# Kernel optimization log

Hardware: AMD Instinct MI355X
Metric: run time of the kernel (lower is better)

The kernel has to match this reference:

```python
import jax, jax.numpy as jnp
import numpy as np


def setup_inputs() -> dict:
    key = jax.random.key(0)
    ks = jax.random.split(key, 5)
    B, M, R = 32, 32, 128
    d_lang, d_region, d_rank, d_fusion = 1024, 2048, 256, 256
    u = jax.random.normal(ks[0], (B, M, d_lang), dtype=jnp.float32)
    v = jax.random.normal(ks[1], (B, R, d_region), dtype=jnp.float32)
    # Linear weights stored torch-style as (out_features, in_features)
    Wu = jax.random.normal(ks[2], (d_rank, d_lang), dtype=jnp.float32) * (1.0 / np.sqrt(d_lang))
    Wv = jax.random.normal(ks[3], (d_rank, d_region), dtype=jnp.float32) * (1.0 / np.sqrt(d_region))
    Wp = jax.random.normal(ks[4], (d_fusion, d_rank), dtype=jnp.float32) * (1.0 / np.sqrt(d_rank))
    bp = jnp.zeros((d_fusion,), dtype=jnp.float32)
    return {"u": u, "v": v, "Wu": Wu, "Wv": Wv, "Wp": Wp, "bp": bp}


def reference(u, v, Wu, Wv, Wp, bp):
    # u: (B, M, d_lang), v: (B, R, d_region)
    up = jnp.einsum('bmd,rd->bmr', u, Wu)          # (B, M, d_rank)  [rd: out x in]
    vp = jnp.einsum('bnd,rd->bnr', v, Wv)          # (B, R, d_rank)
    # broadcast bilinear multiply: (B, M, R, d_rank)
    prod = up[:, :, None, :] * vp[:, None, :, :]
    o = jnp.einsum('bmnk,fk->bmnf', prod, Wp) + bp  # p-linear -> (B, M, R, d_fusion)
    # dropout is identity in inference mode
    return jax.nn.relu(o)
```

## Files before the change

### kernel.cpp

```cpp
#include <hip/hip_runtime.h>
#include <hip/hip_bf16.h>


typedef __attribute__((ext_vector_type(8))) short short8;
typedef __attribute__((ext_vector_type(4))) float floatx4;
typedef __attribute__((ext_vector_type(4))) unsigned uintx4;

__device__ __forceinline__ short f2bf(float f) {
    union { float f; unsigned u; } cv; cv.f = f;
    unsigned r = cv.u + 0x7fffu + ((cv.u >> 16) & 1u);
    return (short)(r >> 16);
}
__device__ __forceinline__ unsigned pack_rne(float x, float y) {
    __hip_bfloat162 h = __float22bfloat162_rn(make_float2(x, y));
    union { __hip_bfloat162 h; unsigned u; } cv; cv.h = h;
    return cv.u;
}
__device__ __forceinline__ unsigned scale2_rne(short a, short b, float ua, float ub) {
    float x = __uint_as_float(((unsigned)(unsigned short)a) << 16) * ua;
    float y = __uint_as_float(((unsigned)(unsigned short)b) << 16) * ub;
    return pack_rne(x, y);
}

#define MFMA16(a, b, c) __builtin_amdgcn_mfma_f32_16x16x32_bf16((a), (b), (c), 0, 0, 0)

__global__ __launch_bounds__(256) void proj_kernel(
    const float* __restrict__ u, const float* __restrict__ Wu,
    float* __restrict__ upf,
    const float* __restrict__ v, const float* __restrict__ Wv,
    short* __restrict__ vpb,
    const float* __restrict__ Wp, short* __restrict__ Wp_bf)
{
    __shared__ __align__(16) short Xs[2][32 * 64];
    __shared__ __align__(16) short Wsh[2][64 * 64];

    const int tid  = threadIdx.x;
    const int lane = tid & 63;
    const int wave = tid >> 6;
    const int quad = lane >> 4;
    const int l15  = lane & 15;

    const int bid = blockIdx.x;

    if (bid < 32) {
        const int widx = (bid * 256 + tid) * 8;
        float4 g0 = *(const float4*)(Wp + widx);
        float4 g1 = *(const float4*)(Wp + widx + 4);
        short8 o;
        o[0] = f2bf(g0.x); o[1] = f2bf(g0.y); o[2] = f2bf(g0.z); o[3] = f2bf(g0.w);
        o[4] = f2bf(g1.x); o[5] = f2bf(g1.y); o[6] = f2bf(g1.z); o[7] = f2bf(g1.w);
        *(short8*)(Wp_bf + widx) = o;
    }

    const int xcd = bid & 7, j = bid >> 3;
    const int cb  = j & 3;
    const int pidx = xcd + 8 * (j >> 2);
    const float *X, *W; int D, r0; bool is_u;
    if (pidx < 32) { is_u = true;  X = u; W = Wu; D = 1024; r0 = pidx * 32; }
    else           { is_u = false; X = v; W = Wv; D = 2048; r0 = (pidx - 32) * 32; }
    const int c0 = cb * 64;
    const int wr = (wave >> 1) * 16;
    const int wc = (wave & 1) * 32;

    const int xr_ = tid >> 3, xk = (tid & 7) * 8;
    const int wr_ = tid >> 2, wk = (tid & 3) * 16;
    const float* xg = X + (size_t)(r0 + xr_) * D + xk;
    const float* wg = W + (size_t)(c0 + wr_) * D + wk;
    const int xswz  = (xr_ & 7) << 4;
    const int wswz  = (wr_ & 7) << 4;
    const int xbase = xr_ * 128 + xk * 2;
    const int wbase = wr_ * 128 + wk * 2;

    floatx4 acc[2] = {};
    float4 x0, x1, y0, y1, y2, y3;

#define LDC(k)                                                                  \
    x0 = *(const float4*)(xg + (k));      x1 = *(const float4*)(xg + (k) + 4);  \
    y0 = *(const float4*)(wg + (k));      y1 = *(const float4*)(wg + (k) + 4);  \
    y2 = *(const float4*)(wg + (k) + 8);  y3 = *(const float4*)(wg + (k) + 12);

#define PKC(bi)                                                                 \
    { char* xb = (char*)&Xs[bi][0]; char* wb = (char*)&Wsh[bi][0]; uintx4 q;    \
      q[0] = pack_rne(x0.x, x0.y); q[1] = pack_rne(x0.z, x0.w);                 \
      q[2] = pack_rne(x1.x, x1.y); q[3] = pack_rne(x1.z, x1.w);                 \
      *(uintx4*)(xb + (xbase ^ xswz)) = q;                                      \
      q[0] = pack_rne(y0.x, y0.y); q[1] = pack_rne(y0.z, y0.w);                 \
      q[2] = pack_rne(y1.x, y1.y); q[3] = pack_rne(y1.z, y1.w);                 \
      *(uintx4*)(wb + (wbase ^ wswz)) = q;                                      \
      q[0] = pack_rne(y2.x, y2.y); q[1] = pack_rne(y2.z, y2.w);                 \
      q[2] = pack_rne(y3.x, y3.y); q[3] = pack_rne(y3.z, y3.w);                 \
      *(uintx4*)(wb + ((wbase + 16) ^ wswz)) = q; }

    LDC(0); PKC(0);
    __syncthreads();

    const int asw = (l15 & 7) << 4;
    int cur = 0;
    for (int kc = 0; kc < D; kc += 64) {
        const bool has = (kc + 64) < D;
        if (has) { LDC(kc + 64); }

        const char* xb = (const char*)&Xs[cur][0];
        const char* wb = (const char*)&Wsh[cur][0];
        short8 a0  = *(const short8*)(xb + (((wr + l15) * 128 +      quad * 16) ^ asw));
        short8 a1  = *(const short8*)(xb + (((wr + l15) * 128 + 64 + quad * 16) ^ asw));
        short8 b00 = *(const short8*)(wb + (((wc +      l15) * 128 +      quad * 16) ^ asw));
        short8 b01 = *(const short8*)(wb + (((wc +      l15) * 128 + 64 + quad * 16) ^ asw));
        short8 b10 = *(const short8*)(wb + (((wc + 16 + l15) * 128 +      quad * 16) ^ asw));
        short8 b11 = *(const short8*)(wb + (((wc + 16 + l15) * 128 + 64 + quad * 16) ^ asw));
        acc[0] = MFMA16(a0, b00, acc[0]);
        acc[1] = MFMA16(a0, b10, acc[1]);
        acc[0] = MFMA16(a1, b01, acc[0]);
        acc[1] = MFMA16(a1, b11, acc[1]);

        if (has) { PKC(cur ^ 1); }
        __syncthreads();
        cur ^= 1;
    }
#undef LDC
#undef PKC

    if (is_u) {
#pragma unroll
        for (int tf = 0; tf < 2; tf++)
#pragma unroll
            for (int r = 0; r < 4; r++) {
                const int row = r0 + wr + quad * 4 + r;
                const int col = c0 + wc + tf * 16 + l15;
                upf[(size_t)row * 256 + col] = acc[tf][r];
            }
    } else {
#pragma unroll
        for (int tf = 0; tf < 2; tf++)
#pragma unroll
            for (int r = 0; r < 4; r++) {
                const int row = r0 + wr + quad * 4 + r;
                const int col = c0 + wc + tf * 16 + l15;
                vpb[(size_t)row * 256 + col] = f2bf(acc[tf][r]);
            }
    }
}

__global__ __launch_bounds__(256) void bilinear_kernel(
    const float* __restrict__ up, const short* __restrict__ vp,
    const short* __restrict__ Wp_bf, const float* __restrict__ bp,
    float* __restrict__ out)
{
    __shared__ __align__(16) short A_lds[128 * 256];
    __shared__ float up_s[256];

    const int tid  = threadIdx.x;
    const int lane = tid & 63;
    const int wave = tid >> 6;
    const int quad = lane >> 4;
    const int l15  = lane & 15;

    const int bid = blockIdx.x;
    const int xcd = bid & 7;
    const int grp = bid >> 3;
    const int s   = grp & 63;
    const int b   = (grp >> 6) * 8 + xcd;
    const int m   = s >> 1;
    const int f_blk = s & 1;
    const int bm  = b * 32 + m;
    const int f0  = f_blk * 128;
    const int wn  = (wave >> 1) * 64;
    const int wf  = (wave & 1) * 64;

    up_s[tid] = up[(size_t)bm * 256 + tid];
    __syncthreads();

    {
        const int jrow = (tid >> 2) * 2;
        const int kseg = (tid & 3) * 64;
        const short* vsrc = vp + (size_t)(b * 128 + jrow) * 256 + kseg;
        char* Ab = (char*)A_lds;
#pragma unroll
        for (int i = 0; i < 8; i++) {
            const float4 ua = *(const float4*)&up_s[kseg + i * 8];
            const float4 ub = *(const float4*)&up_s[kseg + i * 8 + 4];
#pragma unroll
            for (int r = 0; r < 2; r++) {
                short8 vv = *(const short8*)(vsrc + r * 256 + i * 8);
                uintx4 o;
                o[0] = scale2_rne(vv[0], vv[1], ua.x, ua.y);
                o[1] = scale2_rne(vv[2], vv[3], ua.z, ua.w);
                o[2] = scale2_rne(vv[4], vv[5], ub.x, ub.y);
                o[3] = scale2_rne(vv[6], vv[7], ub.z, ub.w);
                const int row = jrow + r;
                const int byte = (row * 512 + (kseg + i * 8) * 2) ^ ((row & 7) << 4);
                *(uintx4*)(Ab + byte) = o;
            }
        }
    }
    __syncthreads();

    floatx4 acc[4][4] = {};
    const char* Ab = (const char*)A_lds;
    const int aswz = (l15 & 7) << 4;
    const short* wq = Wp_bf + (size_t)(f0 + wf + l15) * 256 + quad * 8;

    short8 bcur[4], bnxt[4];
#pragma unroll
    for (int tt = 0; tt < 4; tt++)
        bcur[tt] = *(const short8*)(wq + tt * 4096);

#pragma unroll
    for (int kc = 0; kc < 256; kc += 32) {
        if (kc < 224) {
#pragma unroll
            for (int tt = 0; tt < 4; tt++)
                bnxt[tt] = *(const short8*)(wq + tt * 4096 + kc + 32);
        }
        short8 a[4];
#pragma unroll
        for (int tt = 0; tt < 4; tt++) {
            const int row = wn + tt * 16 + l15;
            a[tt] = *(const short8*)(Ab + ((row * 512 + kc * 2 + quad * 16) ^ aswz));
        }
        __builtin_amdgcn_s_setprio(1);
#pragma unroll
        for (int tn = 0; tn < 4; tn++)
#pragma unroll
            for (int tf = 0; tf < 4; tf++)
                acc[tn][tf] = MFMA16(bcur[tf], a[tn], acc[tn][tf]);
        __builtin_amdgcn_s_setprio(0);
        if (kc < 224) {
#pragma unroll
            for (int tt = 0; tt < 4; tt++) bcur[tt] = bnxt[tt];
        }
    }

    float4 bpv[4];
#pragma unroll
    for (int tf = 0; tf < 4; tf++)
        bpv[tf] = *(const float4*)&bp[f0 + wf + tf * 16 + quad * 4];

    const size_t out_base = (size_t)bm * 128 * 256;
#pragma unroll
    for (int tn = 0; tn < 4; tn++) {
        const int n = wn + tn * 16 + l15;
        float* orow = out + out_base + (size_t)n * 256 + f0 + wf + quad * 4;
#pragma unroll
        for (int tf = 0; tf < 4; tf++) {
            float4 vv;
            vv.x = fmaxf(acc[tn][tf][0] + bpv[tf].x, 0.0f);
            vv.y = fmaxf(acc[tn][tf][1] + bpv[tf].y, 0.0f);
            vv.z = fmaxf(acc[tn][tf][2] + bpv[tf].z, 0.0f);
            vv.w = fmaxf(acc[tn][tf][3] + bpv[tf].w, 0.0f);
            *(float4*)(orow + tf * 16) = vv;
        }
    }
}

extern "C" void kernel_launch(void* const* d_in, const int* in_sizes, int n_in,
                              void* d_out, int out_size, void* d_ws, size_t ws_size,
                              hipStream_t stream) {
    const float* u  = (const float*)d_in[0];
    const float* v  = (const float*)d_in[1];
    const float* Wu = (const float*)d_in[2];
    const float* Wv = (const float*)d_in[3];
    const float* Wp = (const float*)d_in[4];
    const float* bp = (const float*)d_in[5];
    float* out = (float*)d_out;

    float* up_f  = (float*)d_ws;
    short* vp_bf = (short*)(up_f + 262144);
    short* Wp_bf = vp_bf + 1048576;

    proj_kernel<<<dim3(640), dim3(256), 0, stream>>>(
        u, Wu, up_f, v, Wv, vp_bf, Wp, Wp_bf);
    bilinear_kernel<<<dim3(2048), dim3(256), 0, stream>>>(
        up_f, vp_bf, Wp_bf, bp, out);
}
```

Before: 245.5 us.

## Split bilinear tile over N rows instead of F columns, halving LDS

Each block now covers 64 region rows and all 256 fusion columns, where before it covered 128 rows and 128 columns. The scaled A tile in LDS drops from 64KB to 32KB, and launch_bounds requests 4 blocks per CU to raise occupancy. Each block now builds half as much scaled vp per output, which removes the duplicated scaling work the old F split caused. Global vp loads are issued before the first barrier to overlap with the up load. In exchange each wave now streams a different 64-row slice of Wp, and the occupancy hint may cap registers for the 64-float accumulator.

```diff
diff --git a/kernel.cpp b/kernel.cpp
--- a/kernel.cpp
+++ b/kernel.cpp
@@ -141,12 +141,12 @@
     }
 }
 
-__global__ __launch_bounds__(256) void bilinear_kernel(
+__global__ __launch_bounds__(256, 4) void bilinear_kernel(
     const float* __restrict__ up, const short* __restrict__ vp,
     const short* __restrict__ Wp_bf, const float* __restrict__ bp,
     float* __restrict__ out)
 {
-    __shared__ __align__(16) short A_lds[128 * 256];
+    __shared__ __align__(16) short A_lds[64 * 256];
     __shared__ float up_s[256];
 
     const int tid  = threadIdx.x;
@@ -161,36 +161,33 @@
     const int s   = grp & 63;
     const int b   = (grp >> 6) * 8 + xcd;
     const int m   = s >> 1;
-    const int f_blk = s & 1;
+    const int nh  = s & 1;
     const int bm  = b * 32 + m;
-    const int f0  = f_blk * 128;
-    const int wn  = (wave >> 1) * 64;
-    const int wf  = (wave & 1) * 64;
 
     up_s[tid] = up[(size_t)bm * 256 + tid];
+
+    const int kw = wave * 64;
+    const short* vsrc = vp + (size_t)(b * 128 + nh * 64 + lane) * 256 + kw;
+    short8 vv[8];
+#pragma unroll
+    for (int i = 0; i < 8; i++) vv[i] = *(const short8*)(vsrc + i * 8);
+
     __syncthreads();
 
     {
-        const int jrow = (tid >> 2) * 2;
-        const int kseg = (tid & 3) * 64;
-        const short* vsrc = vp + (size_t)(b * 128 + jrow) * 256 + kseg;
         char* Ab = (char*)A_lds;
+        const int rsw   = (lane & 7) << 4;
+        const int rbase = lane * 512 + kw * 2;
 #pragma unroll
         for (int i = 0; i < 8; i++) {
-            const float4 ua = *(const float4*)&up_s[kseg + i * 8];
-            const float4 ub = *(const float4*)&up_s[kseg + i * 8 + 4];
-#pragma unroll
-            for (int r = 0; r < 2; r++) {
-                short8 vv = *(const short8*)(vsrc + r * 256 + i * 8);
-                uintx4 o;
-                o[0] = scale2_rne(vv[0], vv[1], ua.x, ua.y);
-                o[1] = scale2_rne(vv[2], vv[3], ua.z, ua.w);
-                o[2] = scale2_rne(vv[4], vv[5], ub.x, ub.y);
-                o[3] = scale2_rne(vv[6], vv[7], ub.z, ub.w);
-                const int row = jrow + r;
-                const int byte = (row * 512 + (kseg + i * 8) * 2) ^ ((row & 7) << 4);
-                *(uintx4*)(Ab + byte) = o;
-            }
+            const float4 ua = *(const float4*)&up_s[kw + i * 8];
+            const float4 ub = *(const float4*)&up_s[kw + i * 8 + 4];
+            uintx4 o;
+            o[0] = scale2_rne(vv[i][0], vv[i][1], ua.x, ua.y);
+            o[1] = scale2_rne(vv[i][2], vv[i][3], ua.z, ua.w);
+            o[2] = scale2_rne(vv[i][4], vv[i][5], ub.x, ub.y);
+            o[3] = scale2_rne(vv[i][6], vv[i][7], ub.z, ub.w);
+            *(uintx4*)(Ab + ((rbase + i * 16) ^ rsw)) = o;
         }
     }
     __syncthreads();
@@ -198,7 +195,8 @@
     floatx4 acc[4][4] = {};
     const char* Ab = (const char*)A_lds;
     const int aswz = (l15 & 7) << 4;
-    const short* wq = Wp_bf + (size_t)(f0 + wf + l15) * 256 + quad * 8;
+    const int wf   = wave * 64;
+    const short* wq = Wp_bf + (size_t)(wf + l15) * 256 + quad * 8;
 
     short8 bcur[4], bnxt[4];
 #pragma unroll
@@ -215,7 +213,7 @@
         short8 a[4];
 #pragma unroll
         for (int tt = 0; tt < 4; tt++) {
-            const int row = wn + tt * 16 + l15;
+            const int row = tt * 16 + l15;
             a[tt] = *(const short8*)(Ab + ((row * 512 + kc * 2 + quad * 16) ^ aswz));
         }
         __builtin_amdgcn_s_setprio(1);
@@ -234,21 +232,21 @@
     float4 bpv[4];
 #pragma unroll
     for (int tf = 0; tf < 4; tf++)
-        bpv[tf] = *(const float4*)&bp[f0 + wf + tf * 16 + quad * 4];
-
-    const size_t out_base = (size_t)bm * 128 * 256;
+        bpv[tf] = *(const float4*)&bp[wf + tf * 16 + quad * 4];
+
+    const size_t out_base = (size_t)bm * 128 * 256 + (size_t)nh * 64 * 256;
 #pragma unroll
     for (int tn = 0; tn < 4; tn++) {
-        const int n = wn + tn * 16 + l15;
-        float* orow = out + out_base + (size_t)n * 256 + f0 + wf + quad * 4;
+        const int n = tn * 16 + l15;
+        float* orow = out + out_base + (size_t)n * 256 + wf + quad * 4;
 #pragma unroll
         for (int tf = 0; tf < 4; tf++) {
-            float4 vv;
-            vv.x = fmaxf(acc[tn][tf][0] + bpv[tf].x, 0.0f);
-            vv.y = fmaxf(acc[tn][tf][1] + bpv[tf].y, 0.0f);
-            vv.z = fmaxf(acc[tn][tf][2] + bpv[tf].z, 0.0f);
-            vv.w = fmaxf(acc[tn][tf][3] + bpv[tf].w, 0.0f);
-            *(float4*)(orow + tf * 16) = vv;
+            float4 vo;
+            vo.x = fmaxf(acc[tn][tf][0] + bpv[tf].x, 0.0f);
+            vo.y = fmaxf(acc[tn][tf][1] + bpv[tf].y, 0.0f);
+            vo.z = fmaxf(acc[tn][tf][2] + bpv[tf].z, 0.0f);
+            vo.w = fmaxf(acc[tn][tf][3] + bpv[tf].w, 0.0f);
+            *(float4*)(orow + tf * 16) = vo;
         }
     }
 }
```

Measured after the change: 230.8 us. -6.0%, faster.
